# Kernel tuning notes

Hardware: AMD Instinct MI355X
Metric: run time of the kernel (lower is better)

Reference implementation:

```python
import jax, jax.numpy as jnp
import numpy as np

N, IN_F, OUT_F = 10000, 512, 64
ALPHA = 0.2       # leaky relu slope
THRESHOLD = 0.01  # hub threshold
NEG_INF = -9.0e15


def setup_inputs() -> dict:
    key = jax.random.key(0)
    k_h, k_adj, k_hub, k_W, k_as, k_ad = jax.random.split(key, 6)
    h = jax.random.normal(k_h, (N, IN_F), dtype=jnp.float32)
    adj = jax.random.randint(k_adj, (N, N), 0, 2, dtype=jnp.int32)
    hub_mask = jax.random.uniform(k_hub, (N,), dtype=jnp.float32)
    # xavier-uniform-ish params (gain 1.414)
    lim_W = 1.414 * np.sqrt(6.0 / (IN_F + OUT_F))
    W = jax.random.uniform(k_W, (IN_F, OUT_F), minval=-lim_W, maxval=lim_W, dtype=jnp.float32)
    lim_a = 1.414 * np.sqrt(6.0 / (OUT_F + 1))
    a_src = jax.random.uniform(k_as, (OUT_F, 1), minval=-lim_a, maxval=lim_a, dtype=jnp.float32)
    a_dst = jax.random.uniform(k_ad, (OUT_F, 1), minval=-lim_a, maxval=lim_a, dtype=jnp.float32)
    return {"h": h, "W": W, "a_src": a_src, "a_dst": a_dst, "hub_mask": hub_mask, "adj": adj}


def reference(h, W, a_src, a_dst, hub_mask, adj):
    Wh = h @ W                                  # [N, F_out]
    e_src = Wh @ a_src                          # [N, 1]
    e_dst = Wh @ a_dst                          # [N, 1]
    e = jax.nn.leaky_relu(e_src + e_dst.T, negative_slope=ALPHA)  # [N, N]
    scores = jnp.where(adj > 0, e, jnp.float32(NEG_INF))
    attention = jax.nn.softmax(scores, axis=1)  # row-wise softmax over neighbors
    attention = jax.nn.relu(attention - hub_mask * THRESHOLD)  # hub threshold prune
    # dropout omitted (inference mode / p applied as no-op for deterministic reference)
    h_prime = attention @ Wh                    # [N, F_out]
    return jax.nn.elu(h_prime)                  # concat=True branch
```

## Files before the change

### kernel.cpp

```cpp
#include <hip/hip_runtime.h>
#include <math.h>

#define N_NODES 10000
#define IN_FEAT 512
#define OUT_FEAT 64
#define LRELU_ALPHA 0.2f
#define HUB_THRESH 0.01f
#define BITS_WORDS 320
#define CAND_CAP 1024

#define WH_OFF   0
#define ESRC_OFF 640000
#define EDST_OFF 650000
#define T_OFF    660000
#define LT_OFF   670000

__global__ __launch_bounds__(256) void k1_gemm(
    const float* __restrict__ h, const float* __restrict__ W,
    const float* __restrict__ a_src, const float* __restrict__ a_dst,
    const float* __restrict__ hub, float* __restrict__ ws)
{
    const int bx = blockIdx.x, tid = threadIdx.x;
    if (bx >= 625) {
        const int base = (bx - 625) * 1024;
        #pragma unroll
        for (int e = 0; e < 4; ++e) {
            int idx = base + e * 256 + tid;
            if (idx < N_NODES) {
                float t = hub[idx] * HUB_THRESH;
                ws[T_OFF + idx]  = t;
                ws[LT_OFF + idx] = logf(t);
            }
        }
        return;
    }

    __shared__ __align__(16) float Ws[64 * 64];
    __shared__ __align__(16) float Hs[16 * 64];
    const int col = tid & 63, rg = tid >> 6;
    const int rowBase = bx * 16;
    float acc[4] = {0.f, 0.f, 0.f, 0.f};

    for (int k0 = 0; k0 < IN_FEAT; k0 += 64) {
        const float4* __restrict__ W4 = (const float4*)(W + (size_t)k0 * 64);
        float4* Ws4 = (float4*)Ws;
        #pragma unroll
        for (int t = 0; t < 4; ++t) Ws4[tid + t * 256] = W4[tid + t * 256];
        ((float4*)Hs)[tid] =
            *(const float4*)&h[(size_t)(rowBase + (tid >> 4)) * IN_FEAT + k0 + (tid & 15) * 4];
        __syncthreads();
        #pragma unroll
        for (int k4 = 0; k4 < 16; ++k4) {
            float4 hv0 = *(const float4*)&Hs[(rg + 0)  * 64 + k4 * 4];
            float4 hv1 = *(const float4*)&Hs[(rg + 4)  * 64 + k4 * 4];
            float4 hv2 = *(const float4*)&Hs[(rg + 8)  * 64 + k4 * 4];
            float4 hv3 = *(const float4*)&Hs[(rg + 12) * 64 + k4 * 4];
            float w0 = Ws[(k4 * 4 + 0) * 64 + col];
            float w1 = Ws[(k4 * 4 + 1) * 64 + col];
            float w2 = Ws[(k4 * 4 + 2) * 64 + col];
            float w3 = Ws[(k4 * 4 + 3) * 64 + col];
            acc[0] += hv0.x * w0 + hv0.y * w1 + hv0.z * w2 + hv0.w * w3;
            acc[1] += hv1.x * w0 + hv1.y * w1 + hv1.z * w2 + hv1.w * w3;
            acc[2] += hv2.x * w0 + hv2.y * w1 + hv2.z * w2 + hv2.w * w3;
            acc[3] += hv3.x * w0 + hv3.y * w1 + hv3.z * w2 + hv3.w * w3;
        }
        __syncthreads();
    }

    const float asv = a_src[col], adv = a_dst[col];
    #pragma unroll
    for (int r = 0; r < 4; ++r) {
        int row = rowBase + rg + 4 * r;
        ws[WH_OFF + (size_t)row * 64 + col] = acc[r];
        float s1 = acc[r] * asv, s2 = acc[r] * adv;
        #pragma unroll
        for (int m = 32; m; m >>= 1) {
            s1 += __shfl_xor(s1, m, 64);
            s2 += __shfl_xor(s2, m, 64);
        }
        if (col == 0) {
            ws[ESRC_OFF + row] = s1;
            ws[EDST_OFF + row] = s2;
        }
    }
}

__global__ __launch_bounds__(256) void k2_fused(
    const int* __restrict__ adj, const float* __restrict__ ws,
    float* __restrict__ out)
{
    const int b = blockIdx.x, tid = threadIdx.x;
    const int lane = tid & 63, w = tid >> 6;
    const int i0 = 2 * b, i1 = 2 * b + 1;
    __shared__ unsigned bits[2][BITS_WORDS];
    __shared__ float partA[2][4];
    __shared__ int2  cand[2][CAND_CAP];
    __shared__ int   cnt[2];
    __shared__ float oaccL[2][64];

    const float esrc0 = ws[ESRC_OFF + i0];
    const float esrc1 = ws[ESRC_OFF + i1];
    const float* __restrict__ edst = ws + EDST_OFF;
    const int4* __restrict__ arow0 = (const int4*)(adj + (size_t)i0 * N_NODES);
    const int4* __restrict__ arow1 = (const int4*)(adj + (size_t)i1 * N_NODES);
    float acc0 = 0.f, acc1 = 0.f;

    if (tid < 2) cnt[tid] = 0;
    if (tid < 128) ((float*)oaccL)[tid] = 0.f;

#define PA_BODY(IT, A0, A1, E4)                                              \
    {                                                                        \
        float s, e, ex;                                                      \
        s = esrc0 + (E4).x; e = fmaxf(s, LRELU_ALPHA * s); ex = __expf(e);   \
        if ((A0).x > 0) acc0 += ex;                                          \
        unsigned long long B0 = __ballot((A0).x > 0);                        \
        s = esrc0 + (E4).y; e = fmaxf(s, LRELU_ALPHA * s); ex = __expf(e);   \
        if ((A0).y > 0) acc0 += ex;                                          \
        unsigned long long B1 = __ballot((A0).y > 0);                        \
        s = esrc0 + (E4).z; e = fmaxf(s, LRELU_ALPHA * s); ex = __expf(e);   \
        if ((A0).z > 0) acc0 += ex;                                          \
        unsigned long long B2 = __ballot((A0).z > 0);                        \
        s = esrc0 + (E4).w; e = fmaxf(s, LRELU_ALPHA * s); ex = __expf(e);   \
        if ((A0).w > 0) acc0 += ex;                                          \
        unsigned long long B3 = __ballot((A0).w > 0);                        \
        s = esrc1 + (E4).x; e = fmaxf(s, LRELU_ALPHA * s); ex = __expf(e);   \
        if ((A1).x > 0) acc1 += ex;                                          \
        unsigned long long B4 = __ballot((A1).x > 0);                        \
        s = esrc1 + (E4).y; e = fmaxf(s, LRELU_ALPHA * s); ex = __expf(e);   \
        if ((A1).y > 0) acc1 += ex;                                          \
        unsigned long long B5 = __ballot((A1).y > 0);                        \
        s = esrc1 + (E4).z; e = fmaxf(s, LRELU_ALPHA * s); ex = __expf(e);   \
        if ((A1).z > 0) acc1 += ex;                                          \
        unsigned long long B6 = __ballot((A1).z > 0);                        \
        s = esrc1 + (E4).w; e = fmaxf(s, LRELU_ALPHA * s); ex = __expf(e);   \
        if ((A1).w > 0) acc1 += ex;                                          \
        unsigned long long B7 = __ballot((A1).w > 0);                        \
        if (lane < 8) {                                                      \
            \
            unsigned long long v =                                           \
                (lane & 4) ? ((lane & 2) ? ((lane & 1) ? B7 : B6)            \
                                         : ((lane & 1) ? B5 : B4))           \
                           : ((lane & 2) ? ((lane & 1) ? B3 : B2)            \
                                         : ((lane & 1) ? B1 : B0));          \
            *((unsigned long long*)&bits[lane >> 2][0] +                     \
              ((IT) * 16 + w * 4 + (lane & 3))) = v;                         \
        }                                                                    \
    }

    #pragma unroll 3
    for (int it = 0; it < 9; ++it) {
        int4 a0 = arow0[it * 256 + tid];
        int4 a1 = arow1[it * 256 + tid];
        float4 e4 = *(const float4*)(edst + it * 1024 + tid * 4);
        PA_BODY(it, a0, a1, e4)
    }
    {
        const int j0 = 9216 + tid * 4;
        int4 a0 = make_int4(0, 0, 0, 0), a1 = make_int4(0, 0, 0, 0);
        float4 e4 = make_float4(0.f, 0.f, 0.f, 0.f);
        if (j0 < N_NODES) {
            a0 = arow0[9 * 256 + tid];
            a1 = arow1[9 * 256 + tid];
            e4 = *(const float4*)(edst + j0);
        }
        PA_BODY(9, a0, a1, e4)
    }
#undef PA_BODY

    #pragma unroll
    for (int m = 32; m; m >>= 1) {
        acc0 += __shfl_xor(acc0, m, 64);
        acc1 += __shfl_xor(acc1, m, 64);
    }
    if (lane == 0) { partA[0][w] = acc0; partA[1][w] = acc1; }
    __syncthreads();
    const float l0 = partA[0][0] + partA[0][1] + partA[0][2] + partA[0][3];
    const float l1 = partA[1][0] + partA[1][1] + partA[1][2] + partA[1][3];

    const bool empty0 = (l0 == 0.0f), empty1 = (l1 == 0.0f);
    const float cl0 = empty0 ? 0.0f : logf(l0);
    const float cl1 = empty1 ? 0.0f : logf(l1);
    const float thr0 = cl0 - 0.0625f, thr1 = cl1 - 0.0625f;
    const float invN = 1.0f / (float)N_NODES;
    const float* __restrict__ tarr  = ws + T_OFF;
    const float* __restrict__ ltarr = ws + LT_OFF;
    const float* __restrict__ Wh    = ws + WH_OFF;
    float oacc0 = 0.f, oacc1 = 0.f;
    const unsigned rm0 = empty0 ? 0u : 0xffffffffu;
    const unsigned rm1 = empty1 ? 0u : 0xffffffffu;
    const unsigned lb = lane & 31;

#define PB_TEST(WROW, ESRC, THR, CL, R, ED, LT, JC)                          \
    if (((WROW) >> lb) & 1u) {                                               \
        float s = (ESRC) + (ED);                                             \
        float e = fmaxf(s, LRELU_ALPHA * s);                                 \
        if (e > (THR) + (LT)) {                                    \
            float p = __expf(e - (CL));                      \
            float wgt = p - tarr[JC];                        \
            if (wgt > 0.0f) {                                                \
                int k = atomicAdd(&cnt[R], 1);                               \
                if (k < CAND_CAP) {                                          \
                    cand[R][k] = make_int2((JC), __float_as_int(wgt));       \
                } else {   \
                    const float* whp = Wh + (size_t)(JC) * 64;               \
                    for (int cc = 0; cc < 64; ++cc)                          \
                        atomicAdd(&oaccL[R][cc], wgt * whp[cc]);             \
                }                                                            \
            }                                                                \
        }                                                                    \
    }

    #pragma unroll 2
    for (int it = 0; it < 10; ++it) {
        const int j0 = it * 1024 + tid * 4;
        if (j0 < N_NODES) {
            const int wb = it * 32 + w * 8 + (lane >> 5);
            const unsigned w00 = bits[0][wb + 0] & rm0;
            const unsigned w01 = bits[0][wb + 2] & rm0;
            const unsigned w02 = bits[0][wb + 4] & rm0;
            const unsigned w03 = bits[0][wb + 6] & rm0;
            const unsigned w10 = bits[1][wb + 0] & rm1;
            const unsigned w11 = bits[1][wb + 2] & rm1;
            const unsigned w12 = bits[1][wb + 4] & rm1;
            const unsigned w13 = bits[1][wb + 6] & rm1;
            if (((w00 | w01 | w02 | w03 | w10 | w11 | w12 | w13) >> lb) & 1u) {
                float4 e4  = *(const float4*)(edst + j0);
                float4 lt4 = *(const float4*)(ltarr + j0);
                PB_TEST(w00, esrc0, thr0, cl0, 0, e4.x, lt4.x, j0 + 0)
                PB_TEST(w10, esrc1, thr1, cl1, 1, e4.x, lt4.x, j0 + 0)
                PB_TEST(w01, esrc0, thr0, cl0, 0, e4.y, lt4.y, j0 + 1)
                PB_TEST(w11, esrc1, thr1, cl1, 1, e4.y, lt4.y, j0 + 1)
                PB_TEST(w02, esrc0, thr0, cl0, 0, e4.z, lt4.z, j0 + 2)
                PB_TEST(w12, esrc1, thr1, cl1, 1, e4.z, lt4.z, j0 + 2)
                PB_TEST(w03, esrc0, thr0, cl0, 0, e4.w, lt4.w, j0 + 3)
                PB_TEST(w13, esrc1, thr1, cl1, 1, e4.w, lt4.w, j0 + 3)
            }
        }
        if ((empty0 | empty1) && j0 < N_NODES) {
            float4 t4 = *(const float4*)(tarr + j0);
            #pragma unroll
            for (int c = 0; c < 4; ++c) {
                float tv = (c == 0) ? t4.x : (c == 1) ? t4.y : (c == 2) ? t4.z : t4.w;
                float wv = invN - tv;
                if (wv > 0.0f) {
                    #pragma unroll
                    for (int r = 0; r < 2; ++r) {
                        if (r == 0 ? empty0 : empty1) {
                            int k = atomicAdd(&cnt[r], 1);
                            if (k < CAND_CAP) {
                                cand[r][k] = make_int2(j0 + c, __float_as_int(wv));
                            } else {
                                const float* whp = Wh + (size_t)(j0 + c) * 64;
                                for (int cc = 0; cc < 64; ++cc)
                                    atomicAdd(&oaccL[r][cc], wv * whp[cc]);
                            }
                        }
                    }
                }
            }
        }
    }
#undef PB_TEST

    __syncthreads();
    const int M0 = min(cnt[0], CAND_CAP), M1 = min(cnt[1], CAND_CAP);

    int c0 = w;
    for (; c0 + 12 < M0; c0 += 16) {
        int2 cd0 = cand[0][c0];
        int2 cd1 = cand[0][c0 + 4];
        int2 cd2 = cand[0][c0 + 8];
        int2 cd3 = cand[0][c0 + 12];
        float v0 = Wh[(size_t)cd0.x * 64 + lane];
        float v1 = Wh[(size_t)cd1.x * 64 + lane];
        float v2 = Wh[(size_t)cd2.x * 64 + lane];
        float v3 = Wh[(size_t)cd3.x * 64 + lane];
        oacc0 += __int_as_float(cd0.y) * v0;
        oacc0 += __int_as_float(cd1.y) * v1;
        oacc0 += __int_as_float(cd2.y) * v2;
        oacc0 += __int_as_float(cd3.y) * v3;
    }
    for (; c0 < M0; c0 += 4) {
        int2 cd = cand[0][c0];
        oacc0 += __int_as_float(cd.y) * Wh[(size_t)cd.x * 64 + lane];
    }
    int c1 = w;
    for (; c1 + 12 < M1; c1 += 16) {
        int2 cd0 = cand[1][c1];
        int2 cd1 = cand[1][c1 + 4];
        int2 cd2 = cand[1][c1 + 8];
        int2 cd3 = cand[1][c1 + 12];
        float v0 = Wh[(size_t)cd0.x * 64 + lane];
        float v1 = Wh[(size_t)cd1.x * 64 + lane];
        float v2 = Wh[(size_t)cd2.x * 64 + lane];
        float v3 = Wh[(size_t)cd3.x * 64 + lane];
        oacc1 += __int_as_float(cd0.y) * v0;
        oacc1 += __int_as_float(cd1.y) * v1;
        oacc1 += __int_as_float(cd2.y) * v2;
        oacc1 += __int_as_float(cd3.y) * v3;
    }
    for (; c1 < M1; c1 += 4) {
        int2 cd = cand[1][c1];
        oacc1 += __int_as_float(cd.y) * Wh[(size_t)cd.x * 64 + lane];
    }

    float* partB = (float*)bits;
    partB[tid]       = oacc0;
    partB[256 + tid] = oacc1;
    __syncthreads();
    if (w < 2) {
        const float* pb = partB + w * 256;
        float tot = pb[lane] + pb[64 + lane] + pb[128 + lane] + pb[192 + lane]
                  + oaccL[w][lane];
        out[(size_t)(i0 + w) * 64 + lane] = tot > 0.0f ? tot : expm1f(tot);
    }
}

extern "C" void kernel_launch(void* const* d_in, const int* in_sizes, int n_in,
                              void* d_out, int out_size, void* d_ws, size_t ws_size,
                              hipStream_t stream)
{
    const float* h     = (const float*)d_in[0];
    const float* W     = (const float*)d_in[1];
    const float* a_src = (const float*)d_in[2];
    const float* a_dst = (const float*)d_in[3];
    const float* hub   = (const float*)d_in[4];
    const int*   adj   = (const int*)d_in[5];
    float* ws  = (float*)d_ws;
    float* out = (float*)d_out;

    k1_gemm<<<635, 256, 0, stream>>>(h, W, a_src, a_dst, hub, ws);
    k2_fused<<<N_NODES / 2, 256, 0, stream>>>(adj, ws, out);
}
```

Before: 599.6 us.

## Factor exp of leaky-relu scores into per-node exponentials and prefilter candidates

The exponential of the leaky-relu score is split into exp(esrc)·exp(edst) or exp(0.2·esrc)·exp(0.2·edst), and the per-column exponentials are precomputed in a new prep kernel. The softmax denominator pass then needs only a max and a multiply per element instead of an exp. The pruning test is recast as a comparison of precomputed ratios against per-row thresholds with a slack factor, which avoids a log per candidate. The GEMM is also retiled so each thread computes four output columns with float4 shared-memory loads. Risks are an extra kernel launch, a fourth stream of ws data to read, and possible overflow of exp for large scores.

```diff
diff --git a/kernel.cpp b/kernel.cpp
--- a/kernel.cpp
+++ b/kernel.cpp
@@ -8,80 +8,84 @@
 #define HUB_THRESH 0.01f
 #define BITS_WORDS 320
 #define CAND_CAP 1024
+#define PREF_SLACK 0.9394131f
 
 #define WH_OFF   0
 #define ESRC_OFF 640000
 #define EDST_OFF 650000
 #define T_OFF    660000
-#define LT_OFF   670000
+#define F1_OFF   670000
+#define F2_OFF   680000
+#define AL_OFF   690000
+#define BE_OFF   700000
 
 __global__ __launch_bounds__(256) void k1_gemm(
     const float* __restrict__ h, const float* __restrict__ W,
     const float* __restrict__ a_src, const float* __restrict__ a_dst,
-    const float* __restrict__ hub, float* __restrict__ ws)
+    float* __restrict__ ws)
 {
     const int bx = blockIdx.x, tid = threadIdx.x;
-    if (bx >= 625) {
-        const int base = (bx - 625) * 1024;
-        #pragma unroll
-        for (int e = 0; e < 4; ++e) {
-            int idx = base + e * 256 + tid;
-            if (idx < N_NODES) {
-                float t = hub[idx] * HUB_THRESH;
-                ws[T_OFF + idx]  = t;
-                ws[LT_OFF + idx] = logf(t);
-            }
-        }
-        return;
-    }
-
     __shared__ __align__(16) float Ws[64 * 64];
-    __shared__ __align__(16) float Hs[16 * 64];
-    const int col = tid & 63, rg = tid >> 6;
-    const int rowBase = bx * 16;
-    float acc[4] = {0.f, 0.f, 0.f, 0.f};
+    __shared__ __align__(16) float Hs[16 * 68];
+    const int row_l = tid >> 4;
+    const int q     = tid & 15;
+    const int c4    = q * 4;
+    const int row   = bx * 16 + row_l;
+    float4 acc = make_float4(0.f, 0.f, 0.f, 0.f);
 
     for (int k0 = 0; k0 < IN_FEAT; k0 += 64) {
         const float4* __restrict__ W4 = (const float4*)(W + (size_t)k0 * 64);
         float4* Ws4 = (float4*)Ws;
         #pragma unroll
         for (int t = 0; t < 4; ++t) Ws4[tid + t * 256] = W4[tid + t * 256];
-        ((float4*)Hs)[tid] =
-            *(const float4*)&h[(size_t)(rowBase + (tid >> 4)) * IN_FEAT + k0 + (tid & 15) * 4];
+        *(float4*)&Hs[row_l * 68 + c4] =
+            *(const float4*)&h[(size_t)row * IN_FEAT + k0 + c4];
         __syncthreads();
         #pragma unroll
         for (int k4 = 0; k4 < 16; ++k4) {
-            float4 hv0 = *(const float4*)&Hs[(rg + 0)  * 64 + k4 * 4];
-            float4 hv1 = *(const float4*)&Hs[(rg + 4)  * 64 + k4 * 4];
-            float4 hv2 = *(const float4*)&Hs[(rg + 8)  * 64 + k4 * 4];
-            float4 hv3 = *(const float4*)&Hs[(rg + 12) * 64 + k4 * 4];
-            float w0 = Ws[(k4 * 4 + 0) * 64 + col];
-            float w1 = Ws[(k4 * 4 + 1) * 64 + col];
-            float w2 = Ws[(k4 * 4 + 2) * 64 + col];
-            float w3 = Ws[(k4 * 4 + 3) * 64 + col];
-            acc[0] += hv0.x * w0 + hv0.y * w1 + hv0.z * w2 + hv0.w * w3;
-            acc[1] += hv1.x * w0 + hv1.y * w1 + hv1.z * w2 + hv1.w * w3;
-            acc[2] += hv2.x * w0 + hv2.y * w1 + hv2.z * w2 + hv2.w * w3;
-            acc[3] += hv3.x * w0 + hv3.y * w1 + hv3.z * w2 + hv3.w * w3;
+            float4 hv = *(const float4*)&Hs[row_l * 68 + k4 * 4];
+            float4 w0 = *(const float4*)&Ws[(k4 * 4 + 0) * 64 + c4];
+            float4 w1 = *(const float4*)&Ws[(k4 * 4 + 1) * 64 + c4];
+            float4 w2 = *(const float4*)&Ws[(k4 * 4 + 2) * 64 + c4];
+            float4 w3 = *(const float4*)&Ws[(k4 * 4 + 3) * 64 + c4];
+            acc.x += hv.x * w0.x + hv.y * w1.x + hv.z * w2.x + hv.w * w3.x;
+            acc.y += hv.x * w0.y + hv.y * w1.y + hv.z * w2.y + hv.w * w3.y;
+            acc.z += hv.x * w0.z + hv.y * w1.z + hv.z * w2.z + hv.w * w3.z;
+            acc.w += hv.x * w0.w + hv.y * w1.w + hv.z * w2.w + hv.w * w3.w;
         }
         __syncthreads();
     }
 
-    const float asv = a_src[col], adv = a_dst[col];
+    *(float4*)&ws[WH_OFF + (size_t)row * 64 + c4] = acc;
+    const float4 as4 = *(const float4*)&a_src[c4];
+    const float4 ad4 = *(const float4*)&a_dst[c4];
+    float s1 = acc.x * as4.x + acc.y * as4.y + acc.z * as4.z + acc.w * as4.w;
+    float s2 = acc.x * ad4.x + acc.y * ad4.y + acc.z * ad4.z + acc.w * ad4.w;
     #pragma unroll
-    for (int r = 0; r < 4; ++r) {
-        int row = rowBase + rg + 4 * r;
-        ws[WH_OFF + (size_t)row * 64 + col] = acc[r];
-        float s1 = acc[r] * asv, s2 = acc[r] * adv;
-        #pragma unroll
-        for (int m = 32; m; m >>= 1) {
-            s1 += __shfl_xor(s1, m, 64);
-            s2 += __shfl_xor(s2, m, 64);
-        }
-        if (col == 0) {
-            ws[ESRC_OFF + row] = s1;
-            ws[EDST_OFF + row] = s2;
-        }
+    for (int m = 1; m <= 8; m <<= 1) {
+        s1 += __shfl_xor(s1, m, 64);
+        s2 += __shfl_xor(s2, m, 64);
+    }
+    if (q == 0) {
+        ws[ESRC_OFF + row] = s1;
+        ws[EDST_OFF + row] = s2;
+    }
+}
+
+__global__ __launch_bounds__(256) void k1b_prep(
+    const float* __restrict__ hub, float* __restrict__ ws)
+{
+    const int j = blockIdx.x * 256 + threadIdx.x;
+    if (j < N_NODES) {
+        float ed = ws[EDST_OFF + j];
+        float F1 = __expf(ed);
+        float F2 = __expf(0.2f * ed);
+        float t  = hub[j] * HUB_THRESH;
+        ws[F1_OFF + j] = F1;
+        ws[F2_OFF + j] = F2;
+        ws[T_OFF  + j] = t;
+        ws[AL_OFF + j] = F1 / t;
+        ws[BE_OFF + j] = F2 / t;
     }
 }
 
@@ -100,41 +104,46 @@
 
     const float esrc0 = ws[ESRC_OFF + i0];
     const float esrc1 = ws[ESRC_OFF + i1];
-    const float* __restrict__ edst = ws + EDST_OFF;
-    const int4* __restrict__ arow0 = (const int4*)(adj + (size_t)i0 * N_NODES);
-    const int4* __restrict__ arow1 = (const int4*)(adj + (size_t)i1 * N_NODES);
+    const float E1_0 = __expf(esrc0), E2_0 = __expf(0.2f * esrc0);
+    const float E1_1 = __expf(esrc1), E2_1 = __expf(0.2f * esrc1);
+    const float R0 = E2_0 / E1_0, R1 = E2_1 / E1_1;
+    const int4*   __restrict__ arow0 = (const int4*)(adj + (size_t)i0 * N_NODES);
+    const int4*   __restrict__ arow1 = (const int4*)(adj + (size_t)i1 * N_NODES);
+    const float4* __restrict__ F14   = (const float4*)(ws + F1_OFF);
+    const float4* __restrict__ F24   = (const float4*)(ws + F2_OFF);
     float acc0 = 0.f, acc1 = 0.f;
 
     if (tid < 2) cnt[tid] = 0;
     if (tid < 128) ((float*)oaccL)[tid] = 0.f;
 
-#define PA_BODY(IT, A0, A1, E4)                                              \
+#define PA_BODY(IT, A0v, A1v, F1v, F2v)                                      \
     {                                                                        \
-        float s, e, ex;                                                      \
-        s = esrc0 + (E4).x; e = fmaxf(s, LRELU_ALPHA * s); ex = __expf(e);   \
-        if ((A0).x > 0) acc0 += ex;                                          \
-        unsigned long long B0 = __ballot((A0).x > 0);                        \
-        s = esrc0 + (E4).y; e = fmaxf(s, LRELU_ALPHA * s); ex = __expf(e);   \
-        if ((A0).y > 0) acc0 += ex;                                          \
-        unsigned long long B1 = __ballot((A0).y > 0);                        \
-        s = esrc0 + (E4).z; e = fmaxf(s, LRELU_ALPHA * s); ex = __expf(e);   \
-        if ((A0).z > 0) acc0 += ex;                                          \
-        unsigned long long B2 = __ballot((A0).z > 0);                        \
-        s = esrc0 + (E4).w; e = fmaxf(s, LRELU_ALPHA * s); ex = __expf(e);   \
-        if ((A0).w > 0) acc0 += ex;                                          \
-        unsigned long long B3 = __ballot((A0).w > 0);                        \
-        s = esrc1 + (E4).x; e = fmaxf(s, LRELU_ALPHA * s); ex = __expf(e);   \
-        if ((A1).x > 0) acc1 += ex;                                          \
-        unsigned long long B4 = __ballot((A1).x > 0);                        \
-        s = esrc1 + (E4).y; e = fmaxf(s, LRELU_ALPHA * s); ex = __expf(e);   \
-        if ((A1).y > 0) acc1 += ex;                                          \
-        unsigned long long B5 = __ballot((A1).y > 0);                        \
-        s = esrc1 + (E4).z; e = fmaxf(s, LRELU_ALPHA * s); ex = __expf(e);   \
-        if ((A1).z > 0) acc1 += ex;                                          \
-        unsigned long long B6 = __ballot((A1).z > 0);                        \
-        s = esrc1 + (E4).w; e = fmaxf(s, LRELU_ALPHA * s); ex = __expf(e);   \
-        if ((A1).w > 0) acc1 += ex;                                          \
-        unsigned long long B7 = __ballot((A1).w > 0);                        \
+        float v0, v1;                                                        \
+        unsigned long long B0, B1, B2, B3, B4, B5, B6, B7;                   \
+        v0 = fmaxf((F1v).x, R0 * (F2v).x);                                   \
+        v1 = fmaxf((F1v).x, R1 * (F2v).x);                                   \
+        if ((A0v).x > 0) acc0 += v0;                                         \
+        if ((A1v).x > 0) acc1 += v1;                                         \
+        B0 = __ballot((A0v).x > 0);                                          \
+        B4 = __ballot((A1v).x > 0);                                          \
+        v0 = fmaxf((F1v).y, R0 * (F2v).y);                                   \
+        v1 = fmaxf((F1v).y, R1 * (F2v).y);                                   \
+        if ((A0v).y > 0) acc0 += v0;                                         \
+        if ((A1v).y > 0) acc1 += v1;                                         \
+        B1 = __ballot((A0v).y > 0);                                          \
+        B5 = __ballot((A1v).y > 0);                                          \
+        v0 = fmaxf((F1v).z, R0 * (F2v).z);                                   \
+        v1 = fmaxf((F1v).z, R1 * (F2v).z);                                   \
+        if ((A0v).z > 0) acc0 += v0;                                         \
+        if ((A1v).z > 0) acc1 += v1;                                         \
+        B2 = __ballot((A0v).z > 0);                                          \
+        B6 = __ballot((A1v).z > 0);                                          \
+        v0 = fmaxf((F1v).w, R0 * (F2v).w);                                   \
+        v1 = fmaxf((F1v).w, R1 * (F2v).w);                                   \
+        if ((A0v).w > 0) acc0 += v0;                                         \
+        if ((A1v).w > 0) acc1 += v1;                                         \
+        B3 = __ballot((A0v).w > 0);                                          \
+        B7 = __ballot((A1v).w > 0);                                          \
         if (lane < 8) {                                                      \
             \
             unsigned long long v =                                           \
@@ -149,21 +158,23 @@
 
     #pragma unroll 3
     for (int it = 0; it < 9; ++it) {
-        int4 a0 = arow0[it * 256 + tid];
-        int4 a1 = arow1[it * 256 + tid];
-        float4 e4 = *(const float4*)(edst + it * 1024 + tid * 4);
-        PA_BODY(it, a0, a1, e4)
+        int4   a0 = arow0[it * 256 + tid];
+        int4   a1 = arow1[it * 256 + tid];
+        float4 f1 = F14[it * 256 + tid];
+        float4 f2 = F24[it * 256 + tid];
+        PA_BODY(it, a0, a1, f1, f2)
     }
     {
-        const int j0 = 9216 + tid * 4;
-        int4 a0 = make_int4(0, 0, 0, 0), a1 = make_int4(0, 0, 0, 0);
-        float4 e4 = make_float4(0.f, 0.f, 0.f, 0.f);
-        if (j0 < N_NODES) {
+        const int j0t = 9216 + tid * 4;
+        int4   a0 = make_int4(0, 0, 0, 0), a1 = make_int4(0, 0, 0, 0);
+        float4 f1 = make_float4(0.f, 0.f, 0.f, 0.f), f2 = f1;
+        if (j0t < N_NODES) {
             a0 = arow0[9 * 256 + tid];
             a1 = arow1[9 * 256 + tid];
-            e4 = *(const float4*)(edst + j0);
+            f1 = F14[9 * 256 + tid];
+            f2 = F24[9 * 256 + tid];
         }
-        PA_BODY(9, a0, a1, e4)
+        PA_BODY(9, a0, a1, f1, f2)
     }
 #undef PA_BODY
 
@@ -174,38 +185,40 @@
     }
     if (lane == 0) { partA[0][w] = acc0; partA[1][w] = acc1; }
     __syncthreads();
-    const float l0 = partA[0][0] + partA[0][1] + partA[0][2] + partA[0][3];
-    const float l1 = partA[1][0] + partA[1][1] + partA[1][2] + partA[1][3];
+    const float l0 = E1_0 * (partA[0][0] + partA[0][1] + partA[0][2] + partA[0][3]);
+    const float l1 = E1_1 * (partA[1][0] + partA[1][1] + partA[1][2] + partA[1][3]);
 
     const bool empty0 = (l0 == 0.0f), empty1 = (l1 == 0.0f);
     const float cl0 = empty0 ? 0.0f : logf(l0);
     const float cl1 = empty1 ? 0.0f : logf(l1);
-    const float thr0 = cl0 - 0.0625f, thr1 = cl1 - 0.0625f;
+    const float A0 = PREF_SLACK * l0 / E1_0, B0v = PREF_SLACK * l0 / E2_0;
+    const float A1 = PREF_SLACK * l1 / E1_1, B1v = PREF_SLACK * l1 / E2_1;
     const float invN = 1.0f / (float)N_NODES;
-    const float* __restrict__ tarr  = ws + T_OFF;
-    const float* __restrict__ ltarr = ws + LT_OFF;
-    const float* __restrict__ Wh    = ws + WH_OFF;
+    const float* __restrict__ tarr = ws + T_OFF;
+    const float* __restrict__ edst = ws + EDST_OFF;
+    const float* __restrict__ alp  = ws + AL_OFF;
+    const float* __restrict__ bet  = ws + BE_OFF;
+    const float* __restrict__ Wh   = ws + WH_OFF;
     float oacc0 = 0.f, oacc1 = 0.f;
     const unsigned rm0 = empty0 ? 0u : 0xffffffffu;
     const unsigned rm1 = empty1 ? 0u : 0xffffffffu;
     const unsigned lb = lane & 31;
 
-#define PB_TEST(WROW, ESRC, THR, CL, R, ED, LT, JC)                          \
-    if (((WROW) >> lb) & 1u) {                                               \
-        float s = (ESRC) + (ED);                                             \
+#define PB_TEST(WROW, Athr, Bthr, ESRC, CL, R, ALc, BEc, JC)                 \
+    if ((((WROW) >> lb) & 1u) && ((ALc) > (Athr) || (BEc) > (Bthr))) {       \
+        float ed = edst[JC];                                                 \
+        float s = (ESRC) + ed;                                               \
         float e = fmaxf(s, LRELU_ALPHA * s);                                 \
-        if (e > (THR) + (LT)) {                                    \
-            float p = __expf(e - (CL));                      \
-            float wgt = p - tarr[JC];                        \
-            if (wgt > 0.0f) {                                                \
-                int k = atomicAdd(&cnt[R], 1);                               \
-                if (k < CAND_CAP) {                                          \
-                    cand[R][k] = make_int2((JC), __float_as_int(wgt));       \
-                } else {   \
-                    const float* whp = Wh + (size_t)(JC) * 64;               \
-                    for (int cc = 0; cc < 64; ++cc)                          \
-                        atomicAdd(&oaccL[R][cc], wgt * whp[cc]);             \
-                }                                                            \
+        float p = __expf(e - (CL));                          \
+        float wgt = p - tarr[JC];                            \
+        if (wgt > 0.0f) {                                                    \
+            int k = atomicAdd(&cnt[R], 1);                                   \
+            if (k < CAND_CAP) {                                              \
+                cand[R][k] = make_int2((JC), __float_as_int(wgt));           \
+            } else {      \
+                const float* whp = Wh + (size_t)(JC) * 64;                   \
+                for (int cc = 0; cc < 64; ++cc)                              \
+                    atomicAdd(&oaccL[R][cc], wgt * whp[cc]);                 \
             }                                                                \
         }                                                                    \
     }
@@ -224,16 +237,16 @@
             const unsigned w12 = bits[1][wb + 4] & rm1;
             const unsigned w13 = bits[1][wb + 6] & rm1;
             if (((w00 | w01 | w02 | w03 | w10 | w11 | w12 | w13) >> lb) & 1u) {
-                float4 e4  = *(const float4*)(edst + j0);
-                float4 lt4 = *(const float4*)(ltarr + j0);
-                PB_TEST(w00, esrc0, thr0, cl0, 0, e4.x, lt4.x, j0 + 0)
-                PB_TEST(w10, esrc1, thr1, cl1, 1, e4.x, lt4.x, j0 + 0)
-                PB_TEST(w01, esrc0, thr0, cl0, 0, e4.y, lt4.y, j0 + 1)
-                PB_TEST(w11, esrc1, thr1, cl1, 1, e4.y, lt4.y, j0 + 1)
-                PB_TEST(w02, esrc0, thr0, cl0, 0, e4.z, lt4.z, j0 + 2)
-                PB_TEST(w12, esrc1, thr1, cl1, 1, e4.z, lt4.z, j0 + 2)
-                PB_TEST(w03, esrc0, thr0, cl0, 0, e4.w, lt4.w, j0 + 3)
-                PB_TEST(w13, esrc1, thr1, cl1, 1, e4.w, lt4.w, j0 + 3)
+                float4 al4 = *(const float4*)(alp + j0);
+                float4 be4 = *(const float4*)(bet + j0);
+                PB_TEST(w00, A0, B0v, esrc0, cl0, 0, al4.x, be4.x, j0 + 0)
+                PB_TEST(w10, A1, B1v, esrc1, cl1, 1, al4.x, be4.x, j0 + 0)
+                PB_TEST(w01, A0, B0v, esrc0, cl0, 0, al4.y, be4.y, j0 + 1)
+                PB_TEST(w11, A1, B1v, esrc1, cl1, 1, al4.y, be4.y, j0 + 1)
+                PB_TEST(w02, A0, B0v, esrc0, cl0, 0, al4.z, be4.z, j0 + 2)
+                PB_TEST(w12, A1, B1v, esrc1, cl1, 1, al4.z, be4.z, j0 + 2)
+                PB_TEST(w03, A0, B0v, esrc0, cl0, 0, al4.w, be4.w, j0 + 3)
+                PB_TEST(w13, A1, B1v, esrc1, cl1, 1, al4.w, be4.w, j0 + 3)
             }
         }
         if ((empty0 | empty1) && j0 < N_NODES) {
@@ -329,6 +342,7 @@
     float* ws  = (float*)d_ws;
     float* out = (float*)d_out;
 
-    k1_gemm<<<635, 256, 0, stream>>>(h, W, a_src, a_dst, hub, ws);
+    k1_gemm<<<625, 256, 0, stream>>>(h, W, a_src, a_dst, ws);
+    k1b_prep<<<40, 256, 0, stream>>>(hub, ws);
     k2_fused<<<N_NODES / 2, 256, 0, stream>>>(adj, ws, out);
 }
```

After: 592.0 us. About the same (-1.3%).
